# Performance work log

Measured on AMD Instinct MI355X. Metric: run time of the kernel, lower is better.

Reference implementation:

```python
import jax, jax.numpy as jnp
import numpy as np

B, S, E, H = 8, 1024, 1024, 16
D = E // H          # head_dim = 64
FF = 4 * E          # mlp hidden = 4096
EPS = 1e-5


def setup_inputs() -> dict:
    key = jax.random.key(0)
    ks = jax.random.split(key, 12)
    s_e = 1.0 / np.sqrt(E)
    s_ff = 1.0 / np.sqrt(FF)
    return {
        "x": jax.random.normal(ks[0], (B, S, E), jnp.float32),
        # per-head q/k/v projections stacked: [H, E, D] (math layout: y = x @ W + b)
        "Wq": jax.random.normal(ks[1], (H, E, D), jnp.float32) * s_e,
        "bq": jnp.zeros((H, D), jnp.float32),
        "Wk": jax.random.normal(ks[2], (H, E, D), jnp.float32) * s_e,
        "bk": jnp.zeros((H, D), jnp.float32),
        "Wv": jax.random.normal(ks[3], (H, E, D), jnp.float32) * s_e,
        "bv": jnp.zeros((H, D), jnp.float32),
        # output projection [E, E]
        "Wo": jax.random.normal(ks[4], (E, E), jnp.float32) * s_e,
        "bo": jnp.zeros((E,), jnp.float32),
        # layernorms
        "g1": jnp.ones((E,), jnp.float32),
        "beta1": jnp.zeros((E,), jnp.float32),
        "g2": jnp.ones((E,), jnp.float32),
        "beta2": jnp.zeros((E,), jnp.float32),
        # MLP
        "W1": jax.random.normal(ks[5], (E, FF), jnp.float32) * s_e,
        "c1": jnp.zeros((FF,), jnp.float32),
        "W2": jax.random.normal(ks[6], (FF, E), jnp.float32) * s_ff,
        "c2": jnp.zeros((E,), jnp.float32),
    }


def _layernorm(x, g, b):
    mu = jnp.mean(x, axis=-1, keepdims=True)
    var = jnp.mean(jnp.square(x - mu), axis=-1, keepdims=True)
    return (x - mu) * jax.lax.rsqrt(var + EPS) * g + b


def _block(x, Wq, bq, Wk, bk, Wv, bv, Wo, bo, g1, beta1, g2, beta2, W1, c1, W2, c2):
    # --- attention sublayer (pre-norm) ---
    xn = _layernorm(x, g1, beta1)
    # all heads at once (equivalent to the per-head Python loop)
    q = jnp.einsum("bse,hed->bhsd", xn, Wq) + bq[:, None, :]
    k = jnp.einsum("bse,hed->bhsd", xn, Wk) + bk[:, None, :]
    v = jnp.einsum("bse,hed->bhsd", xn, Wv) + bv[:, None, :]
    scale = D ** -0.5
    scores = jnp.einsum("bhsd,bhtd->bhst", q, k) * scale  # [B,H,S,S]
    w = jax.nn.softmax(scores, axis=-1)
    ctx = jnp.einsum("bhst,bhtd->bhsd", w, v)             # [B,H,S,D]
    ctx = ctx.transpose(0, 2, 1, 3).reshape(x.shape[0], x.shape[1], E)  # concat heads
    attn_out = ctx @ Wo + bo
    x = x + attn_out
    # --- MLP sublayer (pre-norm) ---
    xn = _layernorm(x, g2, beta2)
    h = jax.nn.gelu(xn @ W1 + c1, approximate=False)
    return x + (h @ W2 + c2)


def reference(x, Wq, bq, Wk, bk, Wv, bv, Wo, bo, g1, beta1, g2, beta2, W1, c1, W2, c2):
    return _block(x, Wq, bq, Wk, bk, Wv, bv, Wo, bo, g1, beta1, g2, beta2, W1, c1, W2, c2)
```

## Files before the change

### kernel.cpp

```cpp
#include <hip/hip_runtime.h>
#include <math.h>


typedef _Float16 h16;
typedef __attribute__((ext_vector_type(8))) _Float16 f16x8;
typedef __attribute__((ext_vector_type(4))) float f32x4;

__device__ __forceinline__ void gl2lds16(const void* g, void* l) {
  __builtin_amdgcn_global_load_lds(
      (const __attribute__((address_space(1))) void*)g,
      (__attribute__((address_space(3))) void*)l, 16, 0, 0);
}

__global__ __launch_bounds__(256) void repack_kernel(
    const float* __restrict__ Wq, const float* __restrict__ Wk,
    const float* __restrict__ Wv, const float* __restrict__ Wo,
    const float* __restrict__ W1, const float* __restrict__ W2,
    const float* __restrict__ bq, const float* __restrict__ bk,
    const float* __restrict__ bv,
    h16* __restrict__ WqkvT, h16* __restrict__ WoT, h16* __restrict__ W1T,
    h16* __restrict__ W2T, float* __restrict__ bqkv)
{
  const int t = blockIdx.x;
  const int tid = threadIdx.x;
  if (t == 3072) {
    for (int i = tid; i < 3072; i += 256)
      bqkv[i] = (i < 1024) ? bq[i] : (i < 2048 ? bk[i - 1024] : bv[i - 2048]);
    return;
  }
  __shared__ float ld[64 * 65];

  const float* src; h16* dst;
  int sRS, dRS, k0, sn0, dn0;
  if (t < 768) {
    const int m = t >> 8, tt = t & 255, h = tt >> 4, tk = tt & 15;
    src = ((m == 0) ? Wq : (m == 1) ? Wk : Wv) + (size_t)h * 65536;
    dst = WqkvT; sRS = 64; dRS = 1024;
    k0 = tk * 64; sn0 = 0; dn0 = m * 1024 + h * 64;
  } else if (t < 1024) {
    const int tt = t - 768, tk = tt >> 4, tn = tt & 15;
    src = Wo; dst = WoT; sRS = 1024; dRS = 1024;
    k0 = tk * 64; sn0 = tn * 64; dn0 = tn * 64;
  } else if (t < 2048) {
    const int tt = t - 1024, tk = tt >> 6, tn = tt & 63;
    src = W1; dst = W1T; sRS = 4096; dRS = 1024;
    k0 = tk * 64; sn0 = tn * 64; dn0 = tn * 64;
  } else {
    const int tt = t - 2048, tk = tt >> 4, tn = tt & 15;
    src = W2; dst = W2T; sRS = 1024; dRS = 4096;
    k0 = tk * 64; sn0 = tn * 64; dn0 = tn * 64;
  }

  #pragma unroll
  for (int p = 0; p < 16; ++p) {
    const int idx = p * 256 + tid;
    const int r = idx >> 6, c = idx & 63;
    ld[c * 65 + r] = src[(size_t)(k0 + r) * sRS + sn0 + c];
  }
  __syncthreads();
  #pragma unroll
  for (int p = 0; p < 8; ++p) {
    const int idx = p * 512 + tid * 2;
    const int n = idx >> 6, k = idx & 63;
    union { unsigned int u; h16 e[2]; } pk;
    pk.e[0] = (h16)ld[n * 65 + k];
    pk.e[1] = (h16)ld[n * 65 + k + 1];
    *(unsigned int*)&dst[(size_t)(dn0 + n) * dRS + k0 + k] = pk.u;
  }
}

template <int IT>
__global__ __launch_bounds__(256) void ln_kernel(
    const void* __restrict__ in, const float* __restrict__ gw,
    const float* __restrict__ bw, h16* __restrict__ outp)
{
  const int row = blockIdx.x;
  const int tid = threadIdx.x;
  float v[4];
  if (IT == 0) {
    const float* p = (const float*)in + (size_t)row * 1024 + tid * 4;
    float4 tt = *(const float4*)p;
    v[0] = tt.x; v[1] = tt.y; v[2] = tt.z; v[3] = tt.w;
  } else {
    const h16* p = (const h16*)in + (size_t)row * 1024 + tid * 4;
    union { uint2 u; h16 h[4]; } raw;
    raw.u = *(const uint2*)p;
    v[0] = (float)raw.h[0]; v[1] = (float)raw.h[1];
    v[2] = (float)raw.h[2]; v[3] = (float)raw.h[3];
  }
  float s = v[0] + v[1] + v[2] + v[3];
  float ss = v[0]*v[0] + v[1]*v[1] + v[2]*v[2] + v[3]*v[3];
  #pragma unroll
  for (int off = 32; off >= 1; off >>= 1) {
    s += __shfl_down(s, off);
    ss += __shfl_down(ss, off);
  }
  __shared__ float red[8];
  const int w = tid >> 6;
  if ((tid & 63) == 0) { red[w] = s; red[4 + w] = ss; }
  __syncthreads();
  s = red[0] + red[1] + red[2] + red[3];
  ss = red[4] + red[5] + red[6] + red[7];
  const float mean = s * (1.0f / 1024.0f);
  const float var = ss * (1.0f / 1024.0f) - mean * mean;
  const float inv = rsqrtf(fmaxf(var, 0.0f) + 1e-5f);
  union { uint2 u; h16 h[4]; } pk;
  #pragma unroll
  for (int i = 0; i < 4; ++i)
    pk.h[i] = (h16)((v[i] - mean) * inv * gw[tid * 4 + i] + bw[tid * 4 + i]);
  *(uint2*)(outp + (size_t)row * 1024 + tid * 4) = pk.u;
}

#define GEMM201_LDS 131072

template <int MODE>
__global__ __launch_bounds__(512, 2) void gemm201(
    const h16* __restrict__ A, const h16* __restrict__ BT,
    const float* __restrict__ bias, const void* __restrict__ res,
    void* __restrict__ out, int M, int N, int K)
{
  extern __shared__ __align__(16) char smem[];
  const int tid = threadIdx.x;
  const int lane = tid & 63, w = tid >> 6;
  const int l15 = lane & 15, quad = lane >> 4;
  const int wr = w >> 2, wc = w & 3;
  const int m0 = blockIdx.y * 256, n0 = blockIdx.x * 256;
  const int NI = K >> 7;

  const int sr = tid >> 3;
  const int sk = ((tid & 7) ^ (sr & 7)) * 8;
  const h16* gAs = A + (size_t)(m0 + sr) * K + sk;
  const h16* gBs = BT + (size_t)(n0 + sr) * K + sk;
  const int dst0 = tid * 16;

  const int x7 = l15 & 7;
  const int sw0 = (quad ^ x7) << 4;
  const int sw1 = ((4 + quad) ^ x7) << 4;
  const int aBase = wr * 16384;
  const int bBase = 32768 + (wc >> 1) * 16384;
  const int bRow0 = (wc & 1) * 64;

  f32x4 zero = {0.f, 0.f, 0.f, 0.f};
  f32x4 acc[8][4];
  #pragma unroll
  for (int a = 0; a < 8; ++a)
    #pragma unroll
    for (int b = 0; b < 4; ++b) acc[a][b] = zero;

  f16x8 AF0[4][2], AF1[4][2], BF0[2][2], BF1[2][2];

  auto rdA = [&](int bufo, int mi0, f16x8 (&AF)[4][2]) {
    #pragma unroll
    for (int mi = 0; mi < 4; ++mi) {
      const char* p = smem + bufo + aBase + ((mi0 + mi) * 16 + l15) * 128;
      AF[mi][0] = *(const f16x8*)(p + sw0);
      AF[mi][1] = *(const f16x8*)(p + sw1);
    }
  };
  auto rdB = [&](int bufo, int ni0, f16x8 (&BF)[2][2]) {
    #pragma unroll
    for (int ni = 0; ni < 2; ++ni) {
      const char* p = smem + bufo + bBase + (bRow0 + (ni0 + ni) * 16 + l15) * 128;
      BF[ni][0] = *(const f16x8*)(p + sw0);
      BF[ni][1] = *(const f16x8*)(p + sw1);
    }
  };
  auto mmq = [&](int mi0, int ni0, f16x8 (&AF)[4][2], f16x8 (&BF)[2][2]) {
    __builtin_amdgcn_s_setprio(1);
    #pragma unroll
    for (int mi = 0; mi < 4; ++mi)
      #pragma unroll
      for (int ni = 0; ni < 2; ++ni) {
        acc[mi0 + mi][ni0 + ni] = __builtin_amdgcn_mfma_f32_16x16x32_f16(
            AF[mi][0], BF[ni][0], acc[mi0 + mi][ni0 + ni], 0, 0, 0);
        acc[mi0 + mi][ni0 + ni] = __builtin_amdgcn_mfma_f32_16x16x32_f16(
            AF[mi][1], BF[ni][1], acc[mi0 + mi][ni0 + ni], 0, 0, 0);
      }
    __builtin_amdgcn_s_setprio(0);
  };

#define STG_A(b, h, T) { \
    char* d_ = smem + (b) * 65536 + (h) * 16384 + dst0; \
    const h16* g_ = gAs + (size_t)((h) * 128) * K + (size_t)(T) * 64; \
    gl2lds16(g_, d_); gl2lds16(g_ + (size_t)64 * K, d_ + 8192); }
#define STG_B(b, h, T) { \
    char* d_ = smem + (b) * 65536 + 32768 + (h) * 16384 + dst0; \
    const h16* g_ = gBs + (size_t)((h) * 128) * K + (size_t)(T) * 64; \
    gl2lds16(g_, d_); gl2lds16(g_ + (size_t)64 * K, d_ + 8192); }
#define BAR __builtin_amdgcn_s_barrier()
#define VMC(n) { asm volatile("s_waitcnt vmcnt(" #n ")" ::: "memory"); \
                 __builtin_amdgcn_sched_barrier(0); }

  STG_A(0, 0, 0); STG_A(0, 1, 0); STG_B(0, 0, 0); STG_B(0, 1, 0);
  STG_A(1, 0, 1); STG_A(1, 1, 1); STG_B(1, 0, 1);
  VMC(6);
  BAR;

  for (int i = 0; i < NI - 1; ++i) {
    const int E = 2 * i, O = E + 1;
    rdA(0, 0, AF0); rdB(0, 0, BF0);
    STG_B(1, 1, O);
    BAR; mmq(0, 0, AF0, BF0); BAR;
    rdA(0, 4, AF1);
    BAR; mmq(4, 0, AF1, BF0); BAR;
    rdB(0, 2, BF1);
    STG_A(0, 0, E + 2);
    BAR; mmq(4, 2, AF1, BF1); BAR;
    STG_A(0, 1, E + 2); STG_B(0, 0, E + 2);
    VMC(6);
    BAR; mmq(0, 2, AF0, BF1); BAR;
    rdA(65536, 0, AF0); rdB(65536, 0, BF0);
    STG_B(0, 1, E + 2);
    BAR; mmq(0, 0, AF0, BF0); BAR;
    rdA(65536, 4, AF1);
    BAR; mmq(4, 0, AF1, BF0); BAR;
    rdB(65536, 2, BF1);
    STG_A(1, 0, O + 2);
    BAR; mmq(4, 2, AF1, BF1); BAR;
    STG_A(1, 1, O + 2); STG_B(1, 0, O + 2);
    VMC(6);
    BAR; mmq(0, 2, AF0, BF1); BAR;
  }

  {
    const int O = 2 * NI - 1;
    rdA(0, 0, AF0); rdB(0, 0, BF0);
    STG_B(1, 1, O);
    BAR; mmq(0, 0, AF0, BF0); BAR;
    rdA(0, 4, AF1);
    BAR; mmq(4, 0, AF1, BF0); BAR;
    rdB(0, 2, BF1);
    BAR; mmq(4, 2, AF1, BF1); BAR;
    VMC(0);
    BAR; mmq(0, 2, AF0, BF1); BAR;
    rdA(65536, 0, AF0); rdB(65536, 0, BF0);
    BAR; mmq(0, 0, AF0, BF0); BAR;
    rdA(65536, 4, AF1);
    BAR; mmq(4, 0, AF1, BF0); BAR;
    rdB(65536, 2, BF1);
    BAR; mmq(4, 2, AF1, BF1); BAR;
    mmq(0, 2, AF0, BF1);
  }

  #pragma unroll
  for (int mi = 0; mi < 8; ++mi) {
    #pragma unroll
    for (int ni = 0; ni < 4; ++ni) {
      #pragma unroll
      for (int i = 0; i < 4; ++i) {
        const int r = m0 + wr * 128 + mi * 16 + quad * 4 + i;
        const int c = n0 + wc * 64 + ni * 16 + l15;
        const size_t idx = (size_t)r * N + c;
        float v = acc[mi][ni][i] + bias[c];
        if (MODE == 0) {
          ((h16*)out)[idx] = (h16)v;
        } else if (MODE == 1) {
          v += ((const float*)res)[idx];
          ((h16*)out)[idx] = (h16)v;
        } else if (MODE == 2) {
          const float e = __expf(v * (-1.5957691216f - 0.0713548163f * v * v));
          v = v / (1.0f + e);
          ((h16*)out)[idx] = (h16)v;
        } else {
          v += (float)((const h16*)res)[idx];
          ((float*)out)[idx] = v;
        }
      }
    }
  }
#undef STG_A
#undef STG_B
#undef BAR
#undef VMC
}

#define GEMM_LDS 147456

template <int MODE>
__global__ __launch_bounds__(512, 2) void gemm_bt(
    const h16* __restrict__ A, const h16* __restrict__ BT,
    const float* __restrict__ bias, const void* __restrict__ res,
    void* __restrict__ out, int M, int N, int K)
{
  extern __shared__ __align__(16) char smem[];
  const int tid = threadIdx.x;
  const int lane = tid & 63, w = tid >> 6;
  const int l15 = lane & 15, quad = lane >> 4;
  const int wm = w >> 1, wn = w & 1;
  const int m0 = blockIdx.y * 256, n0 = blockIdx.x * 128;
  const int NT = K >> 6;

  const int srow = w * 8 + (lane >> 3);
  const int scol = ((lane & 7) ^ ((lane >> 3) & 7)) * 8;
  const h16* gA = A + (size_t)(m0 + srow) * K + scol;
  const h16* gB = BT + (size_t)(n0 + srow) * K + scol;
  const int ldsw = w * 1024;

  const int arow = wm * 64 + l15;
  const int brow = wn * 64 + l15;
  const int x7 = l15 & 7;
  const int sw0 = (quad ^ x7) << 4;
  const int sw1 = ((4 | quad) ^ x7) << 4;

  f32x4 zero = {0.f, 0.f, 0.f, 0.f};
  f32x4 acc[4][4];
  #pragma unroll
  for (int a = 0; a < 4; ++a)
    #pragma unroll
    for (int b = 0; b < 4; ++b) acc[a][b] = zero;

  {
    char* b0 = smem;
    char* b1 = smem + 49152;
    #pragma unroll
    for (int j = 0; j < 4; ++j) gl2lds16(gA + (size_t)j * 64 * K, b0 + j * 8192 + ldsw);
    #pragma unroll
    for (int j = 0; j < 2; ++j) gl2lds16(gB + (size_t)j * 64 * K, b0 + 32768 + j * 8192 + ldsw);
    #pragma unroll
    for (int j = 0; j < 4; ++j) gl2lds16(gA + 64 + (size_t)j * 64 * K, b1 + j * 8192 + ldsw);
    #pragma unroll
    for (int j = 0; j < 2; ++j) gl2lds16(gB + 64 + (size_t)j * 64 * K, b1 + 32768 + j * 8192 + ldsw);
  }
  asm volatile("s_waitcnt vmcnt(6)" ::: "memory");
  __builtin_amdgcn_sched_barrier(0);
  __builtin_amdgcn_s_barrier();

  int cur = 0, pre = 2;
  for (int t = 0; t < NT; ++t) {
    const char* Ab = smem + cur * 49152;
    const char* Bb = Ab + 32768;
    char* Pb = smem + pre * 49152;
    const bool pf = (t + 2) < NT;
    f16x8 af[4], af1[4], bf[4][2];

    #pragma unroll
    for (int mi = 0; mi < 4; ++mi)
      af[mi] = *(const f16x8*)(Ab + (arow + mi * 16) * 128 + sw0);
    #pragma unroll
    for (int mi = 0; mi < 4; ++mi)
      af1[mi] = *(const f16x8*)(Ab + (arow + mi * 16) * 128 + sw1);
    #pragma unroll
    for (int ni = 0; ni < 2; ++ni) {
      bf[ni][0] = *(const f16x8*)(Bb + (brow + ni * 16) * 128 + sw0);
      bf[ni][1] = *(const f16x8*)(Bb + (brow + ni * 16) * 128 + sw1);
    }
    if (pf) {
      const h16* g = gA + (size_t)(t + 2) * 64;
      #pragma unroll
      for (int j = 0; j < 4; ++j) gl2lds16(g + (size_t)j * 64 * K, Pb + j * 8192 + ldsw);
    }
    __builtin_amdgcn_s_barrier();
    __builtin_amdgcn_s_setprio(1);
    #pragma unroll
    for (int mi = 0; mi < 4; ++mi)
      #pragma unroll
      for (int ni = 0; ni < 2; ++ni) {
        acc[mi][ni] = __builtin_amdgcn_mfma_f32_16x16x32_f16(af[mi], bf[ni][0], acc[mi][ni], 0, 0, 0);
        acc[mi][ni] = __builtin_amdgcn_mfma_f32_16x16x32_f16(af1[mi], bf[ni][1], acc[mi][ni], 0, 0, 0);
      }
    __builtin_amdgcn_s_setprio(0);
    __builtin_amdgcn_s_barrier();

    #pragma unroll
    for (int ni = 2; ni < 4; ++ni) {
      bf[ni][0] = *(const f16x8*)(Bb + (brow + ni * 16) * 128 + sw0);
      bf[ni][1] = *(const f16x8*)(Bb + (brow + ni * 16) * 128 + sw1);
    }
    if (pf) {
      const h16* g = gB + (size_t)(t + 2) * 64;
      #pragma unroll
      for (int j = 0; j < 2; ++j) gl2lds16(g + (size_t)j * 64 * K, Pb + 32768 + j * 8192 + ldsw);
    }
    __builtin_amdgcn_s_barrier();
    __builtin_amdgcn_s_setprio(1);
    #pragma unroll
    for (int mi = 0; mi < 4; ++mi)
      #pragma unroll
      for (int ni = 2; ni < 4; ++ni) {
        acc[mi][ni] = __builtin_amdgcn_mfma_f32_16x16x32_f16(af[mi], bf[ni][0], acc[mi][ni], 0, 0, 0);
        acc[mi][ni] = __builtin_amdgcn_mfma_f32_16x16x32_f16(af1[mi], bf[ni][1], acc[mi][ni], 0, 0, 0);
      }
    __builtin_amdgcn_s_setprio(0);
    if (pf) {
      asm volatile("s_waitcnt vmcnt(6)" ::: "memory");
    } else if (t + 2 == NT) {
      asm volatile("s_waitcnt vmcnt(0)" ::: "memory");
    }
    __builtin_amdgcn_sched_barrier(0);
    __builtin_amdgcn_s_barrier();
    cur = (cur == 2) ? 0 : cur + 1;
    pre = (pre == 2) ? 0 : pre + 1;
  }

  #pragma unroll
  for (int mi = 0; mi < 4; ++mi) {
    #pragma unroll
    for (int ni = 0; ni < 4; ++ni) {
      #pragma unroll
      for (int i = 0; i < 4; ++i) {
        const int r = m0 + wm * 64 + mi * 16 + quad * 4 + i;
        const int c = n0 + wn * 64 + ni * 16 + l15;
        const size_t idx = (size_t)r * N + c;
        float v = acc[mi][ni][i] + bias[c];
        if (MODE == 0) {
          ((h16*)out)[idx] = (h16)v;
        } else if (MODE == 1) {
          v += ((const float*)res)[idx];
          ((h16*)out)[idx] = (h16)v;
        } else if (MODE == 2) {
          const float e = __expf(v * (-1.5957691216f - 0.0713548163f * v * v));
          v = v / (1.0f + e);
          ((h16*)out)[idx] = (h16)v;
        } else {
          v += (float)((const h16*)res)[idx];
          ((float*)out)[idx] = v;
        }
      }
    }
  }
}

__global__ __launch_bounds__(256, 2) void attn_kernel(
    const h16* __restrict__ qkv, h16* __restrict__ ctx)
{
  const int qb = blockIdx.x;
  const int bh = blockIdx.y;
  const int b = bh >> 4, h = bh & 15;
  const int tid = threadIdx.x;
  const int w = tid >> 6, lane = tid & 63;
  const int l15 = lane & 15, quad = lane >> 4;

  __shared__ __align__(16) h16 Ks[64 * 80];
  __shared__ __align__(16) h16 Vt[64 * 80];
  __shared__ __align__(16) h16 Ps[256 * 80];

  const size_t qrow0 = (size_t)(b * 1024 + qb * 256);
  for (int c = tid; c < 2048; c += 256) {
    const int row = c >> 3, kc = (c & 7) * 8;
    uint4 raw = *(const uint4*)(qkv + (qrow0 + row) * 3072 + h * 64 + kc);
    union { uint4 v; h16 e[8]; } in4, out4;
    in4.v = raw;
    #pragma unroll
    for (int i = 0; i < 8; ++i) out4.e[i] = in4.e[i] * (h16)0.125f;
    *(uint4*)&Ps[row * 80 + kc] = out4.v;
  }
  __syncthreads();
  f16x8 aq[4][2];
  #pragma unroll
  for (int r = 0; r < 4; ++r)
    #pragma unroll
    for (int s = 0; s < 2; ++s)
      aq[r][s] = *(const f16x8*)&Ps[(w * 64 + r * 16 + l15) * 80 + s * 32 + quad * 8];

  f32x4 zero = {0.f, 0.f, 0.f, 0.f};
  f32x4 o_acc[4][4];
  float l_p[4][4];
  #pragma unroll
  for (int r = 0; r < 4; ++r)
    #pragma unroll
    for (int i = 0; i < 4; ++i) { o_acc[r][i] = zero; l_p[r][i] = 0.f; }

  h16* Pw = &Ps[w * 64 * 80];

  for (int jt = 0; jt < 16; ++jt) {
    __syncthreads();
    const size_t kv0 = (size_t)(b * 1024 + jt * 64);
    for (int c = tid; c < 512; c += 256) {
      const int row = c >> 3, kc = (c & 7) * 8;
      *(uint4*)&Ks[row * 80 + kc] =
          *(const uint4*)(qkv + (kv0 + row) * 3072 + 1024 + h * 64 + kc);
    }
    #pragma unroll
    for (int cc = 0; cc < 2; ++cc) {
      const int d0 = (w + cc * 4) * 8;
      uint4 raw = *(const uint4*)(qkv + (kv0 + lane) * 3072 + 2048 + h * 64 + d0);
      union { uint4 v; h16 e[8]; } in4;
      in4.v = raw;
      #pragma unroll
      for (int i = 0; i < 8; ++i) Vt[(d0 + i) * 80 + lane] = in4.e[i];
    }
    __syncthreads();

    f16x8 kf[4][2];
    #pragma unroll
    for (int ni = 0; ni < 4; ++ni)
      #pragma unroll
      for (int s = 0; s < 2; ++s)
        kf[ni][s] = *(const f16x8*)&Ks[(ni * 16 + l15) * 80 + s * 32 + quad * 8];
    #pragma unroll
    for (int r = 0; r < 4; ++r) {
      f32x4 s_acc[4];
      #pragma unroll
      for (int i = 0; i < 4; ++i) s_acc[i] = zero;
      #pragma unroll
      for (int ni = 0; ni < 4; ++ni)
        #pragma unroll
        for (int s = 0; s < 2; ++s)
          s_acc[ni] = __builtin_amdgcn_mfma_f32_16x16x32_f16(aq[r][s], kf[ni][s], s_acc[ni], 0, 0, 0);
      #pragma unroll
      for (int ni = 0; ni < 4; ++ni)
        #pragma unroll
        for (int i = 0; i < 4; ++i) {
          float p = __expf(s_acc[ni][i]);
          l_p[r][i] += p;
          Pw[(r * 16 + quad * 4 + i) * 80 + ni * 16 + l15] = (h16)p;
        }
    }

    f16x8 vf[4][2];
    #pragma unroll
    for (int ni = 0; ni < 4; ++ni)
      #pragma unroll
      for (int s = 0; s < 2; ++s)
        vf[ni][s] = *(const f16x8*)&Vt[(ni * 16 + l15) * 80 + s * 32 + quad * 8];
    #pragma unroll
    for (int r = 0; r < 4; ++r) {
      f16x8 ap0 = *(const f16x8*)&Pw[(r * 16 + l15) * 80 + quad * 8];
      f16x8 ap1 = *(const f16x8*)&Pw[(r * 16 + l15) * 80 + 32 + quad * 8];
      #pragma unroll
      for (int ni = 0; ni < 4; ++ni) {
        o_acc[r][ni] = __builtin_amdgcn_mfma_f32_16x16x32_f16(ap0, vf[ni][0], o_acc[r][ni], 0, 0, 0);
        o_acc[r][ni] = __builtin_amdgcn_mfma_f32_16x16x32_f16(ap1, vf[ni][1], o_acc[r][ni], 0, 0, 0);
      }
    }
  }

  #pragma unroll
  for (int r = 0; r < 4; ++r)
    #pragma unroll
    for (int i = 0; i < 4; ++i) {
      float lt = l_p[r][i];
      #pragma unroll
      for (int off = 1; off < 16; off <<= 1) lt += __shfl_xor(lt, off);
      const float rinv = 1.0f / lt;
      const size_t row = qrow0 + w * 64 + r * 16 + quad * 4 + i;
      #pragma unroll
      for (int ni = 0; ni < 4; ++ni)
        ctx[row * 1024 + h * 64 + ni * 16 + l15] = (h16)(o_acc[r][ni][i] * rinv);
    }
}

extern "C" void kernel_launch(void* const* d_in, const int* in_sizes, int n_in,
                              void* d_out, int out_size, void* d_ws, size_t ws_size,
                              hipStream_t stream) {
  const float* x   = (const float*)d_in[0];
  const float* Wq  = (const float*)d_in[1];
  const float* bq  = (const float*)d_in[2];
  const float* Wk  = (const float*)d_in[3];
  const float* bk  = (const float*)d_in[4];
  const float* Wv  = (const float*)d_in[5];
  const float* bv  = (const float*)d_in[6];
  const float* Wo  = (const float*)d_in[7];
  const float* bo  = (const float*)d_in[8];
  const float* g1  = (const float*)d_in[9];
  const float* be1 = (const float*)d_in[10];
  const float* g2  = (const float*)d_in[11];
  const float* be2 = (const float*)d_in[12];
  const float* W1  = (const float*)d_in[13];
  const float* c1  = (const float*)d_in[14];
  const float* W2  = (const float*)d_in[15];
  const float* c2  = (const float*)d_in[16];

  char* ws = (char*)d_ws;
  h16*   WqkvT = (h16*)(ws + 0);
  h16*   WoT   = (h16*)(ws + 6291456);
  h16*   W1T   = (h16*)(ws + 8388608);
  h16*   W2T   = (h16*)(ws + 16777216);
  float* bqkv  = (float*)(ws + 25165824);
  h16*   bufA  = (h16*)(ws + 25178112);
  h16*   qkv   = (h16*)(ws + 41955328);
  h16*   x1    = (h16*)(ws + 41955328);
  h16*   hbuf  = (h16*)(ws + 58732544);

  static bool attr_done = false;
  if (!attr_done) {
    hipFuncSetAttribute((const void*)gemm_bt<1>, hipFuncAttributeMaxDynamicSharedMemorySize, GEMM_LDS);
    hipFuncSetAttribute((const void*)gemm_bt<3>, hipFuncAttributeMaxDynamicSharedMemorySize, GEMM_LDS);
    hipFuncSetAttribute((const void*)gemm201<0>, hipFuncAttributeMaxDynamicSharedMemorySize, GEMM201_LDS);
    hipFuncSetAttribute((const void*)gemm201<2>, hipFuncAttributeMaxDynamicSharedMemorySize, GEMM201_LDS);
    attr_done = true;
  }

  repack_kernel<<<dim3(3073), dim3(256), 0, stream>>>(Wq, Wk, Wv, Wo, W1, W2, bq, bk, bv,
                                                      WqkvT, WoT, W1T, W2T, bqkv);
  ln_kernel<0><<<dim3(8192), dim3(256), 0, stream>>>(x, g1, be1, bufA);
  gemm201<0><<<dim3(12, 32), dim3(512), GEMM201_LDS, stream>>>(bufA, WqkvT, bqkv, nullptr, qkv,
                                                               8192, 3072, 1024);
  attn_kernel<<<dim3(4, 128), dim3(256), 0, stream>>>(qkv, bufA);
  gemm_bt<1><<<dim3(8, 32), dim3(512), GEMM_LDS, stream>>>(bufA, WoT, bo, x, x1,
                                                           8192, 1024, 1024);
  ln_kernel<1><<<dim3(8192), dim3(256), 0, stream>>>(x1, g2, be2, bufA);
  gemm201<2><<<dim3(16, 32), dim3(512), GEMM201_LDS, stream>>>(bufA, W1T, c1, nullptr, hbuf,
                                                               8192, 4096, 1024);
  gemm_bt<3><<<dim3(8, 32), dim3(512), GEMM_LDS, stream>>>(hbuf, W2T, c2, x1, d_out,
                                                           8192, 1024, 4096);
}
```

Measured before the change: 482.9 us.

## Swap MFMA operands for row-contiguous vectorized epilogue and re-stage gemm201 prefetch

Swaps the A and B operands of the MFMA calls so each lane's four accumulator values lie along contiguous columns of one row. This lets the epilogue issue a single vectorized load and store (float4, or four packed halves) per fragment instead of four scalar strided accesses. The gemm201 pipeline is also restaged: all four half-tiles of the next buffer are issued together, and the vmcnt wait moves after the last MMA quarter so the wait overlaps compute. The change adds a new vector-store helper with alignment assumptions and adjusts wait counts, which risks hazards if a count is wrong.

```diff
diff --git a/kernel.cpp b/kernel.cpp
--- a/kernel.cpp
+++ b/kernel.cpp
@@ -111,6 +111,36 @@
   *(uint2*)(outp + (size_t)row * 1024 + tid * 4) = pk.u;
 }
 
+template <int MODE>
+__device__ __forceinline__ void epi_store4(
+    const f32x4& a, const float* __restrict__ bias, const void* __restrict__ res,
+    void* __restrict__ out, size_t idx, int c)
+{
+  const float4 b4 = *(const float4*)&bias[c];
+  float v0 = a[0] + b4.x, v1 = a[1] + b4.y, v2 = a[2] + b4.z, v3 = a[3] + b4.w;
+  if (MODE == 1) {
+    const float4 r4 = *(const float4*)&((const float*)res)[idx];
+    v0 += r4.x; v1 += r4.y; v2 += r4.z; v3 += r4.w;
+  } else if (MODE == 2) {
+    const float e0 = __expf(v0 * (-1.5957691216f - 0.0713548163f * v0 * v0));
+    const float e1 = __expf(v1 * (-1.5957691216f - 0.0713548163f * v1 * v1));
+    const float e2 = __expf(v2 * (-1.5957691216f - 0.0713548163f * v2 * v2));
+    const float e3 = __expf(v3 * (-1.5957691216f - 0.0713548163f * v3 * v3));
+    v0 /= (1.0f + e0); v1 /= (1.0f + e1); v2 /= (1.0f + e2); v3 /= (1.0f + e3);
+  } else if (MODE == 3) {
+    union { uint2 u; h16 h[4]; } r4;
+    r4.u = *(const uint2*)&((const h16*)res)[idx];
+    v0 += (float)r4.h[0]; v1 += (float)r4.h[1];
+    v2 += (float)r4.h[2]; v3 += (float)r4.h[3];
+    float4 o4; o4.x = v0; o4.y = v1; o4.z = v2; o4.w = v3;
+    *(float4*)&((float*)out)[idx] = o4;
+    return;
+  }
+  union { uint2 u; h16 h[4]; } pk;
+  pk.h[0] = (h16)v0; pk.h[1] = (h16)v1; pk.h[2] = (h16)v2; pk.h[3] = (h16)v3;
+  *(uint2*)&((h16*)out)[idx] = pk.u;
+}
+
 #define GEMM201_LDS 131072
 
 template <int MODE>
@@ -172,9 +202,9 @@
       #pragma unroll
       for (int ni = 0; ni < 2; ++ni) {
         acc[mi0 + mi][ni0 + ni] = __builtin_amdgcn_mfma_f32_16x16x32_f16(
-            AF[mi][0], BF[ni][0], acc[mi0 + mi][ni0 + ni], 0, 0, 0);
+            BF[ni][0], AF[mi][0], acc[mi0 + mi][ni0 + ni], 0, 0, 0);
         acc[mi0 + mi][ni0 + ni] = __builtin_amdgcn_mfma_f32_16x16x32_f16(
-            AF[mi][1], BF[ni][1], acc[mi0 + mi][ni0 + ni], 0, 0, 0);
+            BF[ni][1], AF[mi][1], acc[mi0 + mi][ni0 + ni], 0, 0, 0);
       }
     __builtin_amdgcn_s_setprio(0);
   };
@@ -192,47 +222,46 @@
                  __builtin_amdgcn_sched_barrier(0); }
 
   STG_A(0, 0, 0); STG_A(0, 1, 0); STG_B(0, 0, 0); STG_B(0, 1, 0);
-  STG_A(1, 0, 1); STG_A(1, 1, 1); STG_B(1, 0, 1);
-  VMC(6);
+  STG_A(1, 0, 1); STG_A(1, 1, 1); STG_B(1, 0, 1); STG_B(1, 1, 1);
+  VMC(8);
   BAR;
 
   for (int i = 0; i < NI - 1; ++i) {
     const int E = 2 * i, O = E + 1;
     rdA(0, 0, AF0); rdB(0, 0, BF0);
-    STG_B(1, 1, O);
     BAR; mmq(0, 0, AF0, BF0); BAR;
     rdA(0, 4, AF1);
     BAR; mmq(4, 0, AF1, BF0); BAR;
     rdB(0, 2, BF1);
     STG_A(0, 0, E + 2);
     BAR; mmq(4, 2, AF1, BF1); BAR;
-    STG_A(0, 1, E + 2); STG_B(0, 0, E + 2);
-    VMC(6);
-    BAR; mmq(0, 2, AF0, BF1); BAR;
+    STG_A(0, 1, E + 2); STG_B(0, 0, E + 2); STG_B(0, 1, E + 2);
+    BAR; mmq(0, 2, AF0, BF1);
+    VMC(8);
+    BAR;
     rdA(65536, 0, AF0); rdB(65536, 0, BF0);
-    STG_B(0, 1, E + 2);
     BAR; mmq(0, 0, AF0, BF0); BAR;
     rdA(65536, 4, AF1);
     BAR; mmq(4, 0, AF1, BF0); BAR;
     rdB(65536, 2, BF1);
     STG_A(1, 0, O + 2);
     BAR; mmq(4, 2, AF1, BF1); BAR;
-    STG_A(1, 1, O + 2); STG_B(1, 0, O + 2);
-    VMC(6);
-    BAR; mmq(0, 2, AF0, BF1); BAR;
+    STG_A(1, 1, O + 2); STG_B(1, 0, O + 2); STG_B(1, 1, O + 2);
+    BAR; mmq(0, 2, AF0, BF1);
+    VMC(8);
+    BAR;
   }
 
   {
-    const int O = 2 * NI - 1;
     rdA(0, 0, AF0); rdB(0, 0, BF0);
-    STG_B(1, 1, O);
     BAR; mmq(0, 0, AF0, BF0); BAR;
     rdA(0, 4, AF1);
     BAR; mmq(4, 0, AF1, BF0); BAR;
     rdB(0, 2, BF1);
     BAR; mmq(4, 2, AF1, BF1); BAR;
+    BAR; mmq(0, 2, AF0, BF1);
     VMC(0);
-    BAR; mmq(0, 2, AF0, BF1); BAR;
+    BAR;
     rdA(65536, 0, AF0); rdB(65536, 0, BF0);
     BAR; mmq(0, 0, AF0, BF0); BAR;
     rdA(65536, 4, AF1);
@@ -244,28 +273,11 @@
 
   #pragma unroll
   for (int mi = 0; mi < 8; ++mi) {
+    const int r = m0 + wr * 128 + mi * 16 + l15;
     #pragma unroll
     for (int ni = 0; ni < 4; ++ni) {
-      #pragma unroll
-      for (int i = 0; i < 4; ++i) {
-        const int r = m0 + wr * 128 + mi * 16 + quad * 4 + i;
-        const int c = n0 + wc * 64 + ni * 16 + l15;
-        const size_t idx = (size_t)r * N + c;
-        float v = acc[mi][ni][i] + bias[c];
-        if (MODE == 0) {
-          ((h16*)out)[idx] = (h16)v;
-        } else if (MODE == 1) {
-          v += ((const float*)res)[idx];
-          ((h16*)out)[idx] = (h16)v;
-        } else if (MODE == 2) {
-          const float e = __expf(v * (-1.5957691216f - 0.0713548163f * v * v));
-          v = v / (1.0f + e);
-          ((h16*)out)[idx] = (h16)v;
-        } else {
-          v += (float)((const h16*)res)[idx];
-          ((float*)out)[idx] = v;
-        }
-      }
+      const int c = n0 + wc * 64 + ni * 16 + quad * 4;
+      epi_store4<MODE>(acc[mi][ni], bias, res, out, (size_t)r * N + c, c);
     }
   }
 #undef STG_A
@@ -355,8 +367,8 @@
     for (int mi = 0; mi < 4; ++mi)
       #pragma unroll
       for (int ni = 0; ni < 2; ++ni) {
-        acc[mi][ni] = __builtin_amdgcn_mfma_f32_16x16x32_f16(af[mi], bf[ni][0], acc[mi][ni], 0, 0, 0);
-        acc[mi][ni] = __builtin_amdgcn_mfma_f32_16x16x32_f16(af1[mi], bf[ni][1], acc[mi][ni], 0, 0, 0);
+        acc[mi][ni] = __builtin_amdgcn_mfma_f32_16x16x32_f16(bf[ni][0], af[mi], acc[mi][ni], 0, 0, 0);
+        acc[mi][ni] = __builtin_amdgcn_mfma_f32_16x16x32_f16(bf[ni][1], af1[mi], acc[mi][ni], 0, 0, 0);
       }
     __builtin_amdgcn_s_setprio(0);
     __builtin_amdgcn_s_barrier();
@@ -377,8 +389,8 @@
     for (int mi = 0; mi < 4; ++mi)
       #pragma unroll
       for (int ni = 2; ni < 4; ++ni) {
-        acc[mi][ni] = __builtin_amdgcn_mfma_f32_16x16x32_f16(af[mi], bf[ni][0], acc[mi][ni], 0, 0, 0);
-        acc[mi][ni] = __builtin_amdgcn_mfma_f32_16x16x32_f16(af1[mi], bf[ni][1], acc[mi][ni], 0, 0, 0);
+        acc[mi][ni] = __builtin_amdgcn_mfma_f32_16x16x32_f16(bf[ni][0], af[mi], acc[mi][ni], 0, 0, 0);
+        acc[mi][ni] = __builtin_amdgcn_mfma_f32_16x16x32_f16(bf[ni][1], af1[mi], acc[mi][ni], 0, 0, 0);
       }
     __builtin_amdgcn_s_setprio(0);
     if (pf) {
@@ -394,28 +406,11 @@
 
   #pragma unroll
   for (int mi = 0; mi < 4; ++mi) {
+    const int r = m0 + wm * 64 + mi * 16 + l15;
     #pragma unroll
     for (int ni = 0; ni < 4; ++ni) {
-      #pragma unroll
-      for (int i = 0; i < 4; ++i) {
-        const int r = m0 + wm * 64 + mi * 16 + quad * 4 + i;
-        const int c = n0 + wn * 64 + ni * 16 + l15;
-        const size_t idx = (size_t)r * N + c;
-        float v = acc[mi][ni][i] + bias[c];
-        if (MODE == 0) {
-          ((h16*)out)[idx] = (h16)v;
-        } else if (MODE == 1) {
-          v += ((const float*)res)[idx];
-          ((h16*)out)[idx] = (h16)v;
-        } else if (MODE == 2) {
-          const float e = __expf(v * (-1.5957691216f - 0.0713548163f * v * v));
-          v = v / (1.0f + e);
-          ((h16*)out)[idx] = (h16)v;
-        } else {
-          v += (float)((const h16*)res)[idx];
-          ((float*)out)[idx] = v;
-        }
-      }
+      const int c = n0 + wn * 64 + ni * 16 + quad * 4;
+      epi_store4<MODE>(acc[mi][ni], bias, res, out, (size_t)r * N + c, c);
     }
   }
 }
```

New measurement: 507.4 us. 5.1% more time.

## Replace N=1024 GEMMs with double-buffered quadrant-interleaved gemm201n kernel

Applied to the files above, without the earlier changes.

Replaces the triple-buffered gemm_bt used for the output projection and second MLP GEMM with a new kernel. The new kernel uses two 48KB LDS buffers, processes two K-tiles per loop iteration, and splits each tile into four quadrant MFMA phases with staggered global-to-LDS staging and fragment reuse, mirroring the existing gemm201 schedule. The aim is to overlap loads with MFMA more finely and to cut LDS use from 144KB to 96KB. The cost is more barriers and a reliance on the BAR/VMC macros defined earlier.

```diff
diff --git a/kernel.cpp b/kernel.cpp
--- a/kernel.cpp
+++ b/kernel.cpp
@@ -270,14 +270,12 @@
   }
 #undef STG_A
 #undef STG_B
-#undef BAR
-#undef VMC
 }
 
-#define GEMM_LDS 147456
+#define GEMM201N_LDS 98304
 
 template <int MODE>
-__global__ __launch_bounds__(512, 2) void gemm_bt(
+__global__ __launch_bounds__(512, 2) void gemm201n(
     const h16* __restrict__ A, const h16* __restrict__ BT,
     const float* __restrict__ bias, const void* __restrict__ res,
     void* __restrict__ out, int M, int N, int K)
@@ -286,21 +284,21 @@
   const int tid = threadIdx.x;
   const int lane = tid & 63, w = tid >> 6;
   const int l15 = lane & 15, quad = lane >> 4;
-  const int wm = w >> 1, wn = w & 1;
+  const int wr = w >> 1, wc = w & 1;
   const int m0 = blockIdx.y * 256, n0 = blockIdx.x * 128;
-  const int NT = K >> 6;
-
-  const int srow = w * 8 + (lane >> 3);
-  const int scol = ((lane & 7) ^ ((lane >> 3) & 7)) * 8;
-  const h16* gA = A + (size_t)(m0 + srow) * K + scol;
-  const h16* gB = BT + (size_t)(n0 + srow) * K + scol;
-  const int ldsw = w * 1024;
-
-  const int arow = wm * 64 + l15;
-  const int brow = wn * 64 + l15;
+  const int NI = K >> 7;
+
+  const int sr = tid >> 3;
+  const int sk = ((tid & 7) ^ (sr & 7)) * 8;
+  const h16* gAs = A + (size_t)(m0 + sr) * K + sk;
+  const h16* gBs = BT + (size_t)(n0 + sr) * K + sk;
+  const int dst0 = tid * 16;
+
   const int x7 = l15 & 7;
   const int sw0 = (quad ^ x7) << 4;
-  const int sw1 = ((4 | quad) ^ x7) << 4;
+  const int sw1 = ((4 + quad) ^ x7) << 4;
+  const int aBase = wr * 8192;
+  const int bBase = 32768 + wc * 8192;
 
   f32x4 zero = {0.f, 0.f, 0.f, 0.f};
   f32x4 acc[4][4];
@@ -309,87 +307,96 @@
     #pragma unroll
     for (int b = 0; b < 4; ++b) acc[a][b] = zero;
 
-  {
-    char* b0 = smem;
-    char* b1 = smem + 49152;
-    #pragma unroll
-    for (int j = 0; j < 4; ++j) gl2lds16(gA + (size_t)j * 64 * K, b0 + j * 8192 + ldsw);
-    #pragma unroll
-    for (int j = 0; j < 2; ++j) gl2lds16(gB + (size_t)j * 64 * K, b0 + 32768 + j * 8192 + ldsw);
-    #pragma unroll
-    for (int j = 0; j < 4; ++j) gl2lds16(gA + 64 + (size_t)j * 64 * K, b1 + j * 8192 + ldsw);
-    #pragma unroll
-    for (int j = 0; j < 2; ++j) gl2lds16(gB + 64 + (size_t)j * 64 * K, b1 + 32768 + j * 8192 + ldsw);
-  }
-  asm volatile("s_waitcnt vmcnt(6)" ::: "memory");
-  __builtin_amdgcn_sched_barrier(0);
-  __builtin_amdgcn_s_barrier();
-
-  int cur = 0, pre = 2;
-  for (int t = 0; t < NT; ++t) {
-    const char* Ab = smem + cur * 49152;
-    const char* Bb = Ab + 32768;
-    char* Pb = smem + pre * 49152;
-    const bool pf = (t + 2) < NT;
-    f16x8 af[4], af1[4], bf[4][2];
-
-    #pragma unroll
-    for (int mi = 0; mi < 4; ++mi)
-      af[mi] = *(const f16x8*)(Ab + (arow + mi * 16) * 128 + sw0);
-    #pragma unroll
-    for (int mi = 0; mi < 4; ++mi)
-      af1[mi] = *(const f16x8*)(Ab + (arow + mi * 16) * 128 + sw1);
+  f16x8 AF0[2][2], AF1[2][2], BF0[2][2], BF1[2][2];
+
+  auto rdA = [&](int bufo, int mi0, f16x8 (&AF)[2][2]) {
+    #pragma unroll
+    for (int mi = 0; mi < 2; ++mi) {
+      const char* p = smem + bufo + aBase + ((mi0 + mi) * 16 + l15) * 128;
+      AF[mi][0] = *(const f16x8*)(p + sw0);
+      AF[mi][1] = *(const f16x8*)(p + sw1);
+    }
+  };
+  auto rdB = [&](int bufo, int ni0, f16x8 (&BF)[2][2]) {
     #pragma unroll
     for (int ni = 0; ni < 2; ++ni) {
-      bf[ni][0] = *(const f16x8*)(Bb + (brow + ni * 16) * 128 + sw0);
-      bf[ni][1] = *(const f16x8*)(Bb + (brow + ni * 16) * 128 + sw1);
-    }
-    if (pf) {
-      const h16* g = gA + (size_t)(t + 2) * 64;
-      #pragma unroll
-      for (int j = 0; j < 4; ++j) gl2lds16(g + (size_t)j * 64 * K, Pb + j * 8192 + ldsw);
-    }
-    __builtin_amdgcn_s_barrier();
+      const char* p = smem + bufo + bBase + ((ni0 + ni) * 16 + l15) * 128;
+      BF[ni][0] = *(const f16x8*)(p + sw0);
+      BF[ni][1] = *(const f16x8*)(p + sw1);
+    }
+  };
+  auto mmq = [&](int mi0, int ni0, f16x8 (&AF)[2][2], f16x8 (&BF)[2][2]) {
     __builtin_amdgcn_s_setprio(1);
     #pragma unroll
-    for (int mi = 0; mi < 4; ++mi)
+    for (int mi = 0; mi < 2; ++mi)
       #pragma unroll
       for (int ni = 0; ni < 2; ++ni) {
-        acc[mi][ni] = __builtin_amdgcn_mfma_f32_16x16x32_f16(af[mi], bf[ni][0], acc[mi][ni], 0, 0, 0);
-        acc[mi][ni] = __builtin_amdgcn_mfma_f32_16x16x32_f16(af1[mi], bf[ni][1], acc[mi][ni], 0, 0, 0);
+        acc[mi0 + mi][ni0 + ni] = __builtin_amdgcn_mfma_f32_16x16x32_f16(
+            AF[mi][0], BF[ni][0], acc[mi0 + mi][ni0 + ni], 0, 0, 0);
+        acc[mi0 + mi][ni0 + ni] = __builtin_amdgcn_mfma_f32_16x16x32_f16(
+            AF[mi][1], BF[ni][1], acc[mi0 + mi][ni0 + ni], 0, 0, 0);
       }
     __builtin_amdgcn_s_setprio(0);
-    __builtin_amdgcn_s_barrier();
-
-    #pragma unroll
-    for (int ni = 2; ni < 4; ++ni) {
-      bf[ni][0] = *(const f16x8*)(Bb + (brow + ni * 16) * 128 + sw0);
-      bf[ni][1] = *(const f16x8*)(Bb + (brow + ni * 16) * 128 + sw1);
-    }
-    if (pf) {
-      const h16* g = gB + (size_t)(t + 2) * 64;
-      #pragma unroll
-      for (int j = 0; j < 2; ++j) gl2lds16(g + (size_t)j * 64 * K, Pb + 32768 + j * 8192 + ldsw);
-    }
-    __builtin_amdgcn_s_barrier();
-    __builtin_amdgcn_s_setprio(1);
-    #pragma unroll
-    for (int mi = 0; mi < 4; ++mi)
-      #pragma unroll
-      for (int ni = 2; ni < 4; ++ni) {
-        acc[mi][ni] = __builtin_amdgcn_mfma_f32_16x16x32_f16(af[mi], bf[ni][0], acc[mi][ni], 0, 0, 0);
-        acc[mi][ni] = __builtin_amdgcn_mfma_f32_16x16x32_f16(af1[mi], bf[ni][1], acc[mi][ni], 0, 0, 0);
-      }
-    __builtin_amdgcn_s_setprio(0);
-    if (pf) {
-      asm volatile("s_waitcnt vmcnt(6)" ::: "memory");
-    } else if (t + 2 == NT) {
-      asm volatile("s_waitcnt vmcnt(0)" ::: "memory");
-    }
-    __builtin_amdgcn_sched_barrier(0);
-    __builtin_amdgcn_s_barrier();
-    cur = (cur == 2) ? 0 : cur + 1;
-    pre = (pre == 2) ? 0 : pre + 1;
+  };
+
+#define STG_A(b, h, T) { \
+    char* d_ = smem + (b) * 49152 + (h) * 16384 + dst0; \
+    const h16* g_ = gAs + (size_t)((h) * 128) * K + (size_t)(T) * 64; \
+    gl2lds16(g_, d_); gl2lds16(g_ + (size_t)64 * K, d_ + 8192); }
+#define STG_B(b, h, T) { \
+    char* d_ = smem + (b) * 49152 + 32768 + (h) * 8192 + dst0; \
+    const h16* g_ = gBs + (size_t)((h) * 64) * K + (size_t)(T) * 64; \
+    gl2lds16(g_, d_); }
+
+  STG_A(0, 0, 0); STG_A(0, 1, 0); STG_B(0, 0, 0); STG_B(0, 1, 0);
+  STG_A(1, 0, 1); STG_A(1, 1, 1); STG_B(1, 0, 1);
+  VMC(5);
+  BAR;
+
+  for (int i = 0; i < NI - 1; ++i) {
+    const int E = 2 * i, O = E + 1;
+    rdA(0, 0, AF0); rdB(0, 0, BF0);
+    STG_B(1, 1, O);
+    BAR; mmq(0, 0, AF0, BF0); BAR;
+    rdA(0, 2, AF1);
+    BAR; mmq(2, 0, AF1, BF0); BAR;
+    rdB(0, 2, BF1);
+    STG_A(0, 0, E + 2);
+    BAR; mmq(2, 2, AF1, BF1); BAR;
+    STG_A(0, 1, E + 2); STG_B(0, 0, E + 2);
+    VMC(5);
+    BAR; mmq(0, 2, AF0, BF1); BAR;
+    rdA(49152, 0, AF0); rdB(49152, 0, BF0);
+    STG_B(0, 1, E + 2);
+    BAR; mmq(0, 0, AF0, BF0); BAR;
+    rdA(49152, 2, AF1);
+    BAR; mmq(2, 0, AF1, BF0); BAR;
+    rdB(49152, 2, BF1);
+    STG_A(1, 0, O + 2);
+    BAR; mmq(2, 2, AF1, BF1); BAR;
+    STG_A(1, 1, O + 2); STG_B(1, 0, O + 2);
+    VMC(5);
+    BAR; mmq(0, 2, AF0, BF1); BAR;
+  }
+
+  {
+    const int O = 2 * NI - 1;
+    rdA(0, 0, AF0); rdB(0, 0, BF0);
+    STG_B(1, 1, O);
+    BAR; mmq(0, 0, AF0, BF0); BAR;
+    rdA(0, 2, AF1);
+    BAR; mmq(2, 0, AF1, BF0); BAR;
+    rdB(0, 2, BF1);
+    BAR; mmq(2, 2, AF1, BF1); BAR;
+    VMC(0);
+    BAR; mmq(0, 2, AF0, BF1); BAR;
+    rdA(49152, 0, AF0); rdB(49152, 0, BF0);
+    BAR; mmq(0, 0, AF0, BF0); BAR;
+    rdA(49152, 2, AF1);
+    BAR; mmq(2, 0, AF1, BF0); BAR;
+    rdB(49152, 2, BF1);
+    BAR; mmq(2, 2, AF1, BF1); BAR;
+    mmq(0, 2, AF0, BF1);
   }
 
   #pragma unroll
@@ -398,8 +405,8 @@
     for (int ni = 0; ni < 4; ++ni) {
       #pragma unroll
       for (int i = 0; i < 4; ++i) {
-        const int r = m0 + wm * 64 + mi * 16 + quad * 4 + i;
-        const int c = n0 + wn * 64 + ni * 16 + l15;
+        const int r = m0 + wr * 64 + mi * 16 + quad * 4 + i;
+        const int c = n0 + wc * 64 + ni * 16 + l15;
         const size_t idx = (size_t)r * N + c;
         float v = acc[mi][ni][i] + bias[c];
         if (MODE == 0) {
@@ -418,6 +425,10 @@
       }
     }
   }
+#undef STG_A
+#undef STG_B
+#undef BAR
+#undef VMC
 }
 
 __global__ __launch_bounds__(256, 2) void attn_kernel(
@@ -574,10 +585,10 @@
 
   static bool attr_done = false;
   if (!attr_done) {
-    hipFuncSetAttribute((const void*)gemm_bt<1>, hipFuncAttributeMaxDynamicSharedMemorySize, GEMM_LDS);
-    hipFuncSetAttribute((const void*)gemm_bt<3>, hipFuncAttributeMaxDynamicSharedMemorySize, GEMM_LDS);
     hipFuncSetAttribute((const void*)gemm201<0>, hipFuncAttributeMaxDynamicSharedMemorySize, GEMM201_LDS);
     hipFuncSetAttribute((const void*)gemm201<2>, hipFuncAttributeMaxDynamicSharedMemorySize, GEMM201_LDS);
+    hipFuncSetAttribute((const void*)gemm201n<1>, hipFuncAttributeMaxDynamicSharedMemorySize, GEMM201N_LDS);
+    hipFuncSetAttribute((const void*)gemm201n<3>, hipFuncAttributeMaxDynamicSharedMemorySize, GEMM201N_LDS);
     attr_done = true;
   }
 
@@ -587,11 +598,11 @@
   gemm201<0><<<dim3(12, 32), dim3(512), GEMM201_LDS, stream>>>(bufA, WqkvT, bqkv, nullptr, qkv,
                                                                8192, 3072, 1024);
   attn_kernel<<<dim3(4, 128), dim3(256), 0, stream>>>(qkv, bufA);
-  gemm_bt<1><<<dim3(8, 32), dim3(512), GEMM_LDS, stream>>>(bufA, WoT, bo, x, x1,
-                                                           8192, 1024, 1024);
+  gemm201n<1><<<dim3(8, 32), dim3(512), GEMM201N_LDS, stream>>>(bufA, WoT, bo, x, x1,
+                                                                8192, 1024, 1024);
   ln_kernel<1><<<dim3(8192), dim3(256), 0, stream>>>(x1, g2, be2, bufA);
   gemm201<2><<<dim3(16, 32), dim3(512), GEMM201_LDS, stream>>>(bufA, W1T, c1, nullptr, hbuf,
                                                                8192, 4096, 1024);
-  gemm_bt<3><<<dim3(8, 32), dim3(512), GEMM_LDS, stream>>>(hbuf, W2T, c2, x1, d_out,
-                                                           8192, 1024, 4096);
+  gemm201n<3><<<dim3(8, 32), dim3(512), GEMM201N_LDS, stream>>>(hbuf, W2T, c2, x1, d_out,
+                                                                8192, 1024, 4096);
 }
```

Result: no change. 486.1 us (+0.7%).
